# Performance work log

Measured on AMD Instinct MI355X. Metric: run time of the kernel, lower is better.

The kernel has to match this reference:

```python
import jax, jax.numpy as jnp
import numpy as np

N_NODES = 50000
N_EDGES = 500000
IN_DIM = 32
HID = 64
NUM_GRAPHS = 64


def _inv(d):
    # 1/d with inf -> 0, as in PyG HypergraphConv
    return jnp.where(d > 0, 1.0 / d, 0.0)


def hypergraph_conv(xh, row0, row1, W, b, n_hnodes, n_hedges):
    """PyG HypergraphConv (heads=1, no attention, unit hyperedge weights).
    xh: (n_hnodes, din) hyper-node features; row0: hyper-node ids, row1: hyperedge ids.
    Index n_hnodes / n_hedges is a padding slot for masked-out incidences.
    """
    xw = xh @ W                                   # (n_hnodes, dout) Theta
    xw = jnp.concatenate([xw, jnp.zeros((1, xw.shape[1]), xw.dtype)], axis=0)
    ones = jnp.ones(row0.shape[0], xw.dtype)
    D = _inv(jax.ops.segment_sum(ones, row0, num_segments=n_hnodes + 1))  # node degree^-1
    B = _inv(jax.ops.segment_sum(ones, row1, num_segments=n_hedges + 1))  # edge size^-1
    # node -> hyperedge aggregation, scaled by B
    he = jax.ops.segment_sum(xw[row0], row1, num_segments=n_hedges + 1) * B[:, None]
    # hyperedge -> node aggregation, scaled by D
    out = jax.ops.segment_sum(he[row1], row0, num_segments=n_hnodes + 1) * D[:, None]
    return out[:n_hnodes] + b


def setup_inputs() -> dict:
    key = jax.random.key(0)
    ks = jax.random.split(key, 12)
    x = jax.random.normal(ks[0], (N_NODES, 16), jnp.float32)
    edge_attr = jax.random.normal(ks[1], (N_EDGES, IN_DIM), jnp.float32)
    edge_index = jax.random.randint(ks[2], (2, N_EDGES), 0, N_NODES, dtype=jnp.int64)
    batch = jnp.sort(jax.random.randint(ks[3], (N_NODES,), 0, NUM_GRAPHS, dtype=jnp.int64))
    node_imp = jax.random.uniform(ks[4], (N_NODES,), jnp.float32)
    s = 0.05
    W0 = jax.random.normal(ks[5], (IN_DIM, HID), jnp.float32) * s
    b0 = jax.random.normal(ks[6], (HID,), jnp.float32) * s
    W1 = jax.random.normal(ks[7], (HID, HID), jnp.float32) * s
    b1 = jax.random.normal(ks[8], (HID,), jnp.float32) * s
    W2 = jax.random.normal(ks[9], (HID, HID), jnp.float32) * s
    b2 = jax.random.normal(ks[10], (HID,), jnp.float32) * s
    return {"x": x, "edge_attr": edge_attr, "edge_index": edge_index, "batch": batch,
            "node_imp": node_imp, "W0": W0, "b0": b0, "W1": W1, "b1": b1,
            "W2": W2, "b2": b2, "num_graphs": NUM_GRAPHS}


def reference(x, edge_attr, edge_index, batch, node_imp, W0, b0, W1, b1, W2, b2, num_graphs):
    N = x.shape[0]
    E = edge_index.shape[1]
    edge_imp = jnp.minimum(node_imp[edge_index[0]], node_imp[edge_index[1]])
    # --- Dual Hypergraph Transform (get_DHT) ---
    row0 = jnp.repeat(jnp.arange(E), 2)            # hyper-node = original edge id
    row1 = edge_index.T.reshape(-1)                # hyperedge  = original node id
    deg = jax.ops.segment_sum(jnp.ones(2 * E, jnp.float32), row1, num_segments=N)
    keep = deg[row1] != 1.0                        # drop incidences of degree-1 hyperedges
    row0 = jnp.where(keep, row0, E)                # redirect dropped entries to padding slot
    row1 = jnp.where(keep, row1, N + E)
    # self-loops: hyperedge ids N..N+E-1 (equivalent to torch's max_edge+1.., since
    # unused hyperedge slots receive nothing and B^-1 there is 0)
    row0 = jnp.concatenate([row0, jnp.arange(E)])
    row1 = jnp.concatenate([row1, N + jnp.arange(E)])
    edge_batch = batch[edge_index[0]]              # == hyperedge_index[1].reshape(-1,2)[:,0]
    # --- conv stack (dropout in eval mode = identity) ---
    h = edge_attr * edge_imp[:, None]
    xs = []
    for (W, b) in ((W0, b0), (W1, b1), (W2, b2)):
        h = jax.nn.relu(hypergraph_conv(h, row0, row1, W, b, E, N + E))
        h = h * edge_imp[:, None]
        xs.append(h)
    gh = jnp.concatenate(
        [jax.ops.segment_sum(h_i, edge_batch, num_segments=num_graphs) for h_i in xs], axis=1)
    return gh
```

## Files before the change

### kernel.cpp

```cpp
#include <hip/hip_runtime.h>
#include <hip/hip_bf16.h>
#include <cstdint>
#include <cstddef>

typedef unsigned short u16;
typedef unsigned int   u32;
typedef short bf16x8 __attribute__((ext_vector_type(8)));
typedef float f32x4  __attribute__((ext_vector_type(4)));

__device__ __forceinline__ float bf2f(u16 v){ return __uint_as_float(((u32)v)<<16); }
__device__ __forceinline__ u16 f2bf(float f){
  u32 x = __float_as_uint(f);
  return (u16)((x + 0x7FFFu + ((x>>16)&1u)) >> 16);
}
__device__ __forceinline__ void atomAddF(float* p, float v){ unsafeAtomicAdd(p, v); }
__device__ __forceinline__ float rlanef(float v, int q){
  return __int_as_float(__builtin_amdgcn_readlane(__float_as_int(v), q));
}

__global__ void kzero(int* p, int n){
  int i = blockIdx.x*blockDim.x + threadIdx.x;
  if(i < n) p[i] = 0;
}

__global__ void kdeg2(const int* __restrict__ ei0, const int* __restrict__ ei1,
                      int* __restrict__ deg0, int* __restrict__ deg1, int E){
  int e = blockIdx.x*blockDim.x + threadIdx.x;
  if(e >= E) return;
  atomicAdd(&deg0[ei0[e]], 1);
  atomicAdd(&deg1[ei1[e]], 1);
}

__global__ __launch_bounds__(256) void ktilesum(const int* __restrict__ deg0,
                                                const int* __restrict__ deg1,
                                                int* __restrict__ tsum,
                                                int N, int nt){
  __shared__ int sh[256];
  const int b = blockIdx.x;
  const int* deg = (b < nt) ? deg0 : deg1;
  const int tile = (b < nt) ? b : b - nt;
  const int t = threadIdx.x;
  const int i = tile*256 + t;
  sh[t] = (i < N) ? deg[i] : 0;
  __syncthreads();
  for(int s = 128; s > 0; s >>= 1){
    if(t < s) sh[t] += sh[t+s];
    __syncthreads();
  }
  if(t == 0) tsum[b] = sh[0];
}
__global__ __launch_bounds__(256) void kmid(int* __restrict__ tsum,
                                            int* __restrict__ off0,
                                            int* __restrict__ off1,
                                            int N, int nt){
  __shared__ int sh[256];
  const int b = blockIdx.x;
  int* ts = tsum + b*nt;
  const int t = threadIdx.x;
  sh[t] = (t < nt) ? ts[t] : 0;
  __syncthreads();
  for(int s = 1; s < 256; s <<= 1){
    int x = (t >= s) ? sh[t-s] : 0;
    __syncthreads();
    sh[t] += x;
    __syncthreads();
  }
  if(t < nt) ts[t] = (t == 0) ? 0 : sh[t-1];
  if(t == 255){ int* off = b ? off1 : off0; off[N] = sh[255]; }
}
__global__ __launch_bounds__(256) void kapply(const int* __restrict__ deg0,
                                              const int* __restrict__ deg1,
                                              const int* __restrict__ tsum,
                                              int* __restrict__ off0,
                                              int* __restrict__ off1,
                                              float* __restrict__ dinv,
                                              int N, int nt){
  __shared__ int sh[256];
  const int b = blockIdx.x;
  const int* deg = (b < nt) ? deg0 : deg1;
  int*       off = (b < nt) ? off0 : off1;
  const int tile = (b < nt) ? b : b - nt;
  const int base = tsum[b];
  const int t = threadIdx.x;
  const int i = tile*256 + t;
  sh[t] = (i < N) ? deg[i] : 0;
  __syncthreads();
  for(int s = 1; s < 256; s <<= 1){
    int x = (t >= s) ? sh[t-s] : 0;
    __syncthreads();
    sh[t] += x;
    __syncthreads();
  }
  if(i < N){
    off[i] = base + ((t == 0) ? 0 : sh[t-1]);
    if(b < nt){
      int d = deg0[i] + deg1[i];
      dinv[i] = (d > 1) ? (1.f/(float)d) : 0.f;
    }
  }
}

__global__ void kperm(const int* __restrict__ ei0, const int* __restrict__ ei1,
                      const float* __restrict__ nimp, const float* __restrict__ dinv,
                      const int* __restrict__ batch, const int* __restrict__ off0,
                      int* __restrict__ cur0, u32* __restrict__ euv,
                      f32x4* __restrict__ coef, unsigned char* __restrict__ ebat,
                      int* __restrict__ orig, float* __restrict__ imp, int E){
  int e = blockIdx.x*blockDim.x + threadIdx.x;
  if(e >= E) return;
  int u = ei0[e], v = ei1[e];
  int pos = off0[u] + atomicAdd(&cur0[u], 1);
  float iu = dinv[u], iv = dinv[v];
  float rc = (iu > 0.f && iv > 0.f) ? (1.f/3.f)
           : ((iu > 0.f || iv > 0.f) ? 0.5f : 1.f);
  float ie = fminf(nimp[u], nimp[v]);
  euv[pos]  = (u32)u | ((u32)v << 16);
  f32x4 c; c.x = rc; c.y = iu*rc; c.z = iv*rc; c.w = ie;
  coef[pos] = c;
  ebat[pos] = (unsigned char)batch[u];
  orig[pos] = e;
  imp[pos]  = ie;
}

__global__ void kfillv(const u32* __restrict__ euv, const int* __restrict__ off1,
                       int* __restrict__ cur1, int* __restrict__ list1, int E){
  int p = blockIdx.x*blockDim.x + threadIdx.x;
  if(p >= E) return;
  int v = (int)(euv[p] >> 16);
  list1[off1[v] + atomicAdd(&cur1[v], 1)] = p;
}

__global__ void kprepw(const float* __restrict__ W0, u16* __restrict__ wf0,
                       const float* __restrict__ W1, u16* __restrict__ wf1,
                       const float* __restrict__ W2, u16* __restrict__ wf2){
  const int b = blockIdx.x;
  const float* W; u16* wf; int NC, sbase;
  if(b == 0){ W = W0; wf = wf0; NC = 1; sbase = 0; }
  else if(b <= 2){ W = W1; wf = wf1; NC = 2; sbase = (b-1)*256; }
  else { W = W2; wf = wf2; NC = 2; sbase = (b-3)*256; }
  int s = sbase + threadIdx.x;
  if(s >= 4*NC*64) return;
  int lane = s & 63;
  int c    = (s >> 6) % NC;
  int tt   = s / (NC*64);
  int n  = tt*16 + (lane & 15);
  int k0 = c*32 + (lane >> 4)*8;
  #pragma unroll
  for(int j = 0; j < 8; j++)
    wf[(size_t)s*8 + j] = f2bf(W[(size_t)(k0 + j)*64 + n]);
}

__global__ __launch_bounds__(256) void kgemm0(const float* __restrict__ srcf,
                                              u16* __restrict__ buf,
                                              const u16* __restrict__ wf,
                                              const float* __restrict__ imp,
                                              const int* __restrict__ orig,
                                              int E){
  const int t    = threadIdx.x;
  const int wv   = t >> 6;
  const int lane = t & 63;
  const int quad = lane >> 4;
  const int l15  = lane & 15;
  const int row0 = blockIdx.x*64 + wv*16;
  if(row0 >= E) return;

  bf16x8 bfr[4];
  #pragma unroll
  for(int i = 0; i < 4; i++)
    bfr[i] = *(const bf16x8*)(wf + ((size_t)i*64 + lane)*8);

  const int myrow = row0 + l15;
  const int oe = orig[myrow];
  const float* s = srcf + (size_t)oe*32 + quad*8;
  const float sc = imp[myrow];
  f32x4 v0 = *(const f32x4*)s;
  f32x4 v1 = *(const f32x4*)(s+4);
  bf16x8 afr;
  afr[0]=(short)f2bf(v0.x*sc); afr[1]=(short)f2bf(v0.y*sc);
  afr[2]=(short)f2bf(v0.z*sc); afr[3]=(short)f2bf(v0.w*sc);
  afr[4]=(short)f2bf(v1.x*sc); afr[5]=(short)f2bf(v1.y*sc);
  afr[6]=(short)f2bf(v1.z*sc); afr[7]=(short)f2bf(v1.w*sc);

  #pragma unroll
  for(int tt = 0; tt < 4; tt++){
    f32x4 a = {0.f,0.f,0.f,0.f};
    a = __builtin_amdgcn_mfma_f32_16x16x32_bf16(afr, bfr[tt], a, 0, 0, 0);
    const int n = tt*16 + l15;
    #pragma unroll
    for(int r = 0; r < 4; r++)
      buf[(size_t)(row0 + quad*4 + r)*64 + n] = f2bf(a[r]);
  }
}

__global__ __launch_bounds__(256) void kagg(const u16* __restrict__ buf,
                                            const int* __restrict__ off0,
                                            const int* __restrict__ off1,
                                            const int* __restrict__ list1,
                                            u16* __restrict__ heb, int N){
  const int t = threadIdx.x, wv = t >> 6, lane = t & 63;
  const int n = blockIdx.x*4 + wv;
  if(n >= N) return;
  const int rsub = lane >> 3, cb = lane & 7;
  float acc[8];
  #pragma unroll
  for(int k = 0; k < 8; k++) acc[k] = 0.f;

  auto accum = [&](uint4 x){
    acc[0] += bf2f((u16)x.x); acc[1] += bf2f((u16)(x.x>>16));
    acc[2] += bf2f((u16)x.y); acc[3] += bf2f((u16)(x.y>>16));
    acc[4] += bf2f((u16)x.z); acc[5] += bf2f((u16)(x.z>>16));
    acc[6] += bf2f((u16)x.w); acc[7] += bf2f((u16)(x.w>>16));
  };
  const uint4 zero4 = {0,0,0,0};

  {
    const int s0 = off0[n], d0 = off0[n+1] - s0;
    const u16* base = buf + (size_t)s0*64;
    int j = 0;
    for(; j + 8 <= d0; j += 8)
      accum(*(const uint4*)(base + (size_t)(j+rsub)*64 + cb*8));
    if(j < d0)
      accum((rsub < d0-j) ? *(const uint4*)(base + (size_t)(j+rsub)*64 + cb*8) : zero4);
  }
  {
    const int s1 = off1[n], d1 = off1[n+1] - s1;
    int j = 0;
    for(; j + 8 <= d1; j += 8){
      int e = list1[s1 + j + rsub];
      accum(*(const uint4*)(buf + (size_t)e*64 + cb*8));
    }
    if(j < d1){
      uint4 x = zero4;
      if(rsub < d1-j){
        int e = list1[s1 + j + rsub];
        x = *(const uint4*)(buf + (size_t)e*64 + cb*8);
      }
      accum(x);
    }
  }
  #pragma unroll
  for(int m = 8; m <= 32; m <<= 1)
    #pragma unroll
    for(int k = 0; k < 8; k++) acc[k] += __shfl_xor(acc[k], m);
  if(rsub == 0){
    u32 o[4];
    #pragma unroll
    for(int k = 0; k < 4; k++)
      o[k] = (u32)f2bf(acc[2*k]) | ((u32)f2bf(acc[2*k+1]) << 16);
    *(uint4*)(heb + (size_t)n*64 + cb*8) = make_uint4(o[0],o[1],o[2],o[3]);
  }
}

template<bool DO_GEMM>
__global__ __launch_bounds__(256, 3) void kfused(u16* __restrict__ buf,
                                                 const u16* __restrict__ heb,
                                                 const u32* __restrict__ euv,
                                                 const f32x4* __restrict__ coef,
                                                 const unsigned char* __restrict__ ebat,
                                                 const float* __restrict__ bias,
                                                 const u16* __restrict__ wf,
                                                 float* __restrict__ ghL,
                                                 int E){
  constexpr int HTSZ = DO_GEMM ? 4*16*72 : 4;
  __shared__ __align__(16) u16 hT[HTSZ];
  const int t = threadIdx.x, wv = t >> 6, lane = t & 63;
  const int quad = lane >> 4, l15 = lane & 15;
  const float bd = bias[lane];

  bf16x8 bfr[8];
  if(DO_GEMM){
    #pragma unroll
    for(int i = 0; i < 8; i++)
      bfr[i] = *(const bf16x8*)(wf + ((size_t)i*64 + lane)*8);
  }

  float pool = 0.f;
  int cur_g = -1;
  const int base = __builtin_amdgcn_readfirstlane((int)(blockIdx.x*256) + wv*64);
  u16* hTw = DO_GEMM ? &hT[wv*1152] : &hT[0];

  u32 uvp = 0; f32x4 cf = {0.f,0.f,0.f,0.f}; int bt = 0;
  if(base < E){
    uvp = euv[base + l15];
    cf  = coef[base + l15];
    bt  = (int)ebat[base + l15];
  }

  #pragma unroll
  for(int it = 0; it < 4; it++){
    const int r0 = base + it*16;
    if(r0 < E){
      u16 bv[16], hu[16], hv[16];
      const u16* bufr = buf + (size_t)r0*64;
      #pragma unroll
      for(int q = 0; q < 16; q++){
        const u32 uv = (u32)__builtin_amdgcn_readlane((int)uvp, q);
        hv[q] = heb[(size_t)(uv >> 16)*64 + lane];
        hu[q] = heb[(size_t)(uv & 0xffffu)*64 + lane];
        bv[q] = bufr[q*64 + lane];
      }
      u32 uvpN = uvp; f32x4 cfN = cf; int btN = bt;
      if(it < 3){
        const int r1 = r0 + 16;
        if(r1 < E){
          uvpN = euv[r1 + l15];
          cfN  = coef[r1 + l15];
          btN  = (int)ebat[r1 + l15];
        }
      }
      const int bFirst = __builtin_amdgcn_readlane(bt, 0);
      const int bLast  = __builtin_amdgcn_readlane(bt, 15);
      if(bFirst != cur_g){
        if(cur_g >= 0) atomAddF(&ghL[cur_g*192 + lane], pool);
        pool = 0.f; cur_g = bFirst;
      }
      if(bFirst == bLast){
        #pragma unroll
        for(int q = 0; q < 16; q++){
          const float rc   = rlanef(cf.x, q);
          const float iurc = rlanef(cf.y, q);
          const float ivrc = rlanef(cf.z, q);
          const float ie   = rlanef(cf.w, q);
          float o = fmaxf(fmaf(bf2f(bv[q]), rc,
                          fmaf(bf2f(hu[q]), iurc,
                          fmaf(bf2f(hv[q]), ivrc, bd))), 0.f) * ie;
          pool += o;
          if(DO_GEMM) hTw[q*72 + lane] = f2bf(o);
        }
      } else {
        #pragma unroll
        for(int q = 0; q < 16; q++){
          const float rc   = rlanef(cf.x, q);
          const float iurc = rlanef(cf.y, q);
          const float ivrc = rlanef(cf.z, q);
          const float ie   = rlanef(cf.w, q);
          const int   bq   = __builtin_amdgcn_readlane(bt, q);
          float o = fmaxf(fmaf(bf2f(bv[q]), rc,
                          fmaf(bf2f(hu[q]), iurc,
                          fmaf(bf2f(hv[q]), ivrc, bd))), 0.f) * ie;
          if(bq != cur_g){
            if(cur_g >= 0) atomAddF(&ghL[cur_g*192 + lane], pool);
            pool = 0.f; cur_g = bq;
          }
          pool += o;
          if(DO_GEMM) hTw[q*72 + lane] = f2bf(o);
        }
      }
      if(DO_GEMM){
        bf16x8 afr0 = *(const bf16x8*)&hTw[l15*72 + quad*8];
        bf16x8 afr1 = *(const bf16x8*)&hTw[l15*72 + 32 + quad*8];
        #pragma unroll
        for(int tt = 0; tt < 4; tt++){
          f32x4 a = {0.f,0.f,0.f,0.f};
          a = __builtin_amdgcn_mfma_f32_16x16x32_bf16(afr0, bfr[tt*2+0], a, 0, 0, 0);
          a = __builtin_amdgcn_mfma_f32_16x16x32_bf16(afr1, bfr[tt*2+1], a, 0, 0, 0);
          const int n = tt*16 + l15;
          #pragma unroll
          for(int r = 0; r < 4; r++)
            buf[(size_t)(r0 + quad*4 + r)*64 + n] = f2bf(a[r]);
        }
      }
      uvp = uvpN; cf = cfN; bt = btN;
    }
  }
  if(cur_g >= 0) atomAddF(&ghL[cur_g*192 + lane], pool);
}

__global__ void kfinal(const float* __restrict__ gh, float* __restrict__ out, int n){
  int i = blockIdx.x*blockDim.x + threadIdx.x;
  if(i < n) out[i] = gh[i];
}

extern "C" void kernel_launch(void* const* d_in, const int* in_sizes, int n_in,
                              void* d_out, int out_size, void* d_ws, size_t ws_size,
                              hipStream_t stream) {
  const float* edge_attr = (const float*)d_in[1];
  const int*   ei        = (const int*)d_in[2];
  const int*   batch     = (const int*)d_in[3];
  const float* nimp      = (const float*)d_in[4];
  const float* Ws[3] = { (const float*)d_in[5], (const float*)d_in[7], (const float*)d_in[9] };
  const float* bs[3] = { (const float*)d_in[6], (const float*)d_in[8], (const float*)d_in[10] };

  const int E = in_sizes[1] / 32;
  const int N = in_sizes[4];
  const int* ei0 = ei;
  const int* ei1 = ei + E;

  char* p = (char*)d_ws;
  auto carve = [&](size_t bytes)->char*{
    char* r = p; p += (bytes + 255) & ~(size_t)255; return r;
  };
  const int nt = (N + 255)/256;
  float* imp   = (float*)carve((size_t)E*4);
  int*   deg0  = (int*)  carve((size_t)4*N*4);
  int*   deg1  = deg0 + N;
  int*   cur0  = deg0 + 2*N;
  int*   cur1  = deg0 + 3*N;
  float* dinv  = (float*)carve((size_t)N*4);
  int*   off0  = (int*)  carve((size_t)(N+1)*4);
  int*   off1  = (int*)  carve((size_t)(N+1)*4);
  int*   tsum  = (int*)  carve((size_t)2*nt*4);
  int*   orig  = (int*)  carve((size_t)E*4);
  int*   list1 = (int*)  carve((size_t)E*4);
  u32*   euv   = (u32*)  carve((size_t)E*4);
  f32x4* coef  = (f32x4*)carve((size_t)E*16);
  unsigned char* ebat = (unsigned char*)carve((size_t)E);
  u16*   heb   = (u16*)  carve((size_t)N*64*2);
  u16*   buf   = (u16*)  carve((size_t)E*64*2);
  float* gh    = (float*)carve((size_t)64*192*4);
  u16*   wfs[3];
  for(int l = 0; l < 3; l++) wfs[l] = (u16*)carve((size_t)4096*2);

  kzero<<<(4*N+255)/256, 256, 0, stream>>>(deg0, 4*N);
  kzero<<<(12288+255)/256, 256, 0, stream>>>((int*)gh, 12288);
  kdeg2<<<(E+255)/256, 256, 0, stream>>>(ei0, ei1, deg0, deg1, E);
  ktilesum<<<2*nt, 256, 0, stream>>>(deg0, deg1, tsum, N, nt);
  kmid<<<2, 256, 0, stream>>>(tsum, off0, off1, N, nt);
  kapply<<<2*nt, 256, 0, stream>>>(deg0, deg1, tsum, off0, off1, dinv, N, nt);
  kperm<<<(E+255)/256, 256, 0, stream>>>(ei0, ei1, nimp, dinv, batch, off0, cur0,
                                         euv, coef, ebat, orig, imp, E);
  kfillv<<<(E+255)/256, 256, 0, stream>>>(euv, off1, cur1, list1, E);
  kprepw<<<5, 256, 0, stream>>>(Ws[0], wfs[0], Ws[1], wfs[1], Ws[2], wfs[2]);

  const int nbG = (E + 63)/64;
  const int nbA = (N + 3)/4;
  const int nbF = (E + 255)/256;

  kgemm0<<<nbG, 256, 0, stream>>>(edge_attr, buf, wfs[0], imp, orig, E);
  kagg<<<nbA, 256, 0, stream>>>(buf, off0, off1, list1, heb, N);
  kfused<true ><<<nbF, 256, 0, stream>>>(buf, heb, euv, coef, ebat, bs[0], wfs[1], gh + 0*64, E);
  kagg<<<nbA, 256, 0, stream>>>(buf, off0, off1, list1, heb, N);
  kfused<true ><<<nbF, 256, 0, stream>>>(buf, heb, euv, coef, ebat, bs[1], wfs[2], gh + 1*64, E);
  kagg<<<nbA, 256, 0, stream>>>(buf, off0, off1, list1, heb, N);
  kfused<false><<<nbF, 256, 0, stream>>>(buf, heb, euv, coef, ebat, bs[2], nullptr, gh + 2*64, E);
  kfinal<<<(12288+255)/256, 256, 0, stream>>>(gh, (float*)d_out, 12288);
}
```

Baseline: 447.5 us.

## Pack per-edge records into one AoS struct and scatter gemm0 outputs via inverse permutation

Per-edge metadata (uv, coefficients, importance, batch id) moves from separate SoA arrays into one 32-byte struct, so kfused fetches it with two 16-byte loads instead of three separate loads. kperm now writes scattered 32-byte records plus an inverse permutation and importance in original edge order. kgemm0 then reads edge_attr contiguously and scatters its output rows, and kfillv reads edge ids directly instead of re-reading packed uv. In exchange, record writes in kperm are larger and scattered, and the kgemm0 output stores become scattered row writes.

Result: faster. 432.5 us (-3.4%).

```diff
diff --git a/kernel.cpp b/kernel.cpp
--- a/kernel.cpp
+++ b/kernel.cpp
@@ -7,6 +7,12 @@
 typedef unsigned int   u32;
 typedef short bf16x8 __attribute__((ext_vector_type(8)));
 typedef float f32x4  __attribute__((ext_vector_type(4)));
+
+struct __align__(16) ERec {
+  u32 uv;
+  float rc, iurc, ivrc;
+  float ie; u32 bat; u32 pad0, pad1;
+};
 
 __device__ __forceinline__ float bf2f(u16 v){ return __uint_as_float(((u32)v)<<16); }
 __device__ __forceinline__ u16 f2bf(float f){
@@ -103,9 +109,8 @@
 __global__ void kperm(const int* __restrict__ ei0, const int* __restrict__ ei1,
                       const float* __restrict__ nimp, const float* __restrict__ dinv,
                       const int* __restrict__ batch, const int* __restrict__ off0,
-                      int* __restrict__ cur0, u32* __restrict__ euv,
-                      f32x4* __restrict__ coef, unsigned char* __restrict__ ebat,
-                      int* __restrict__ orig, float* __restrict__ imp, int E){
+                      int* __restrict__ cur0, ERec* __restrict__ rec,
+                      int* __restrict__ iperm, float* __restrict__ impO, int E){
   int e = blockIdx.x*blockDim.x + threadIdx.x;
   if(e >= E) return;
   int u = ei0[e], v = ei1[e];
@@ -114,20 +119,22 @@
   float rc = (iu > 0.f && iv > 0.f) ? (1.f/3.f)
            : ((iu > 0.f || iv > 0.f) ? 0.5f : 1.f);
   float ie = fminf(nimp[u], nimp[v]);
-  euv[pos]  = (u32)u | ((u32)v << 16);
-  f32x4 c; c.x = rc; c.y = iu*rc; c.z = iv*rc; c.w = ie;
-  coef[pos] = c;
-  ebat[pos] = (unsigned char)batch[u];
-  orig[pos] = e;
-  imp[pos]  = ie;
-}
-
-__global__ void kfillv(const u32* __restrict__ euv, const int* __restrict__ off1,
-                       int* __restrict__ cur1, int* __restrict__ list1, int E){
-  int p = blockIdx.x*blockDim.x + threadIdx.x;
-  if(p >= E) return;
-  int v = (int)(euv[p] >> 16);
-  list1[off1[v] + atomicAdd(&cur1[v], 1)] = p;
+  ERec r;
+  r.uv = (u32)u | ((u32)v << 16);
+  r.rc = rc; r.iurc = iu*rc; r.ivrc = iv*rc;
+  r.ie = ie; r.bat = (u32)batch[u]; r.pad0 = 0; r.pad1 = 0;
+  rec[pos]  = r;
+  iperm[e]  = pos;
+  impO[e]   = ie;
+}
+
+__global__ void kfillv(const int* __restrict__ ei1, const int* __restrict__ iperm,
+                       const int* __restrict__ off1, int* __restrict__ cur1,
+                       int* __restrict__ list1, int E){
+  int e = blockIdx.x*blockDim.x + threadIdx.x;
+  if(e >= E) return;
+  int v = ei1[e];
+  list1[off1[v] + atomicAdd(&cur1[v], 1)] = iperm[e];
 }
 
 __global__ void kprepw(const float* __restrict__ W0, u16* __restrict__ wf0,
@@ -153,8 +160,8 @@
 __global__ __launch_bounds__(256) void kgemm0(const float* __restrict__ srcf,
                                               u16* __restrict__ buf,
                                               const u16* __restrict__ wf,
-                                              const float* __restrict__ imp,
-                                              const int* __restrict__ orig,
+                                              const float* __restrict__ impO,
+                                              const int* __restrict__ iperm,
                                               int E){
   const int t    = threadIdx.x;
   const int wv   = t >> 6;
@@ -170,9 +177,9 @@
     bfr[i] = *(const bf16x8*)(wf + ((size_t)i*64 + lane)*8);
 
   const int myrow = row0 + l15;
-  const int oe = orig[myrow];
-  const float* s = srcf + (size_t)oe*32 + quad*8;
-  const float sc = imp[myrow];
+  const float* s = srcf + (size_t)myrow*32 + quad*8;
+  const float sc = impO[myrow];
+  const int ip = iperm[myrow];
   f32x4 v0 = *(const f32x4*)s;
   f32x4 v1 = *(const f32x4*)(s+4);
   bf16x8 afr;
@@ -181,6 +188,10 @@
   afr[4]=(short)f2bf(v1.x*sc); afr[5]=(short)f2bf(v1.y*sc);
   afr[6]=(short)f2bf(v1.z*sc); afr[7]=(short)f2bf(v1.w*sc);
 
+  int dr[4];
+  #pragma unroll
+  for(int r = 0; r < 4; r++) dr[r] = __shfl(ip, quad*4 + r);
+
   #pragma unroll
   for(int tt = 0; tt < 4; tt++){
     f32x4 a = {0.f,0.f,0.f,0.f};
@@ -188,7 +199,7 @@
     const int n = tt*16 + l15;
     #pragma unroll
     for(int r = 0; r < 4; r++)
-      buf[(size_t)(row0 + quad*4 + r)*64 + n] = f2bf(a[r]);
+      buf[(size_t)dr[r]*64 + n] = f2bf(a[r]);
   }
 }
 
@@ -254,9 +265,7 @@
 template<bool DO_GEMM>
 __global__ __launch_bounds__(256, 3) void kfused(u16* __restrict__ buf,
                                                  const u16* __restrict__ heb,
-                                                 const u32* __restrict__ euv,
-                                                 const f32x4* __restrict__ coef,
-                                                 const unsigned char* __restrict__ ebat,
+                                                 const f32x4* __restrict__ rec4,
                                                  const float* __restrict__ bias,
                                                  const u16* __restrict__ wf,
                                                  float* __restrict__ ghL,
@@ -281,9 +290,11 @@
 
   u32 uvp = 0; f32x4 cf = {0.f,0.f,0.f,0.f}; int bt = 0;
   if(base < E){
-    uvp = euv[base + l15];
-    cf  = coef[base + l15];
-    bt  = (int)ebat[base + l15];
+    f32x4 w0 = rec4[(size_t)(base+l15)*2];
+    f32x4 w1 = rec4[(size_t)(base+l15)*2 + 1];
+    uvp = __float_as_uint(w0.x);
+    cf.x = w0.y; cf.y = w0.z; cf.z = w0.w; cf.w = w1.x;
+    bt  = __float_as_int(w1.y);
   }
 
   #pragma unroll
@@ -303,9 +314,11 @@
       if(it < 3){
         const int r1 = r0 + 16;
         if(r1 < E){
-          uvpN = euv[r1 + l15];
-          cfN  = coef[r1 + l15];
-          btN  = (int)ebat[r1 + l15];
+          f32x4 w0 = rec4[(size_t)(r1+l15)*2];
+          f32x4 w1 = rec4[(size_t)(r1+l15)*2 + 1];
+          uvpN = __float_as_uint(w0.x);
+          cfN.x = w0.y; cfN.y = w0.z; cfN.z = w0.w; cfN.w = w1.x;
+          btN  = __float_as_int(w1.y);
         }
       }
       const int bFirst = __builtin_amdgcn_readlane(bt, 0);
@@ -391,7 +404,6 @@
     char* r = p; p += (bytes + 255) & ~(size_t)255; return r;
   };
   const int nt = (N + 255)/256;
-  float* imp   = (float*)carve((size_t)E*4);
   int*   deg0  = (int*)  carve((size_t)4*N*4);
   int*   deg1  = deg0 + N;
   int*   cur0  = deg0 + 2*N;
@@ -400,11 +412,10 @@
   int*   off0  = (int*)  carve((size_t)(N+1)*4);
   int*   off1  = (int*)  carve((size_t)(N+1)*4);
   int*   tsum  = (int*)  carve((size_t)2*nt*4);
-  int*   orig  = (int*)  carve((size_t)E*4);
+  int*   iperm = (int*)  carve((size_t)E*4);
+  float* impO  = (float*)carve((size_t)E*4);
   int*   list1 = (int*)  carve((size_t)E*4);
-  u32*   euv   = (u32*)  carve((size_t)E*4);
-  f32x4* coef  = (f32x4*)carve((size_t)E*16);
-  unsigned char* ebat = (unsigned char*)carve((size_t)E);
+  ERec*  rec   = (ERec*) carve((size_t)E*sizeof(ERec));
   u16*   heb   = (u16*)  carve((size_t)N*64*2);
   u16*   buf   = (u16*)  carve((size_t)E*64*2);
   float* gh    = (float*)carve((size_t)64*192*4);
@@ -418,20 +429,20 @@
   kmid<<<2, 256, 0, stream>>>(tsum, off0, off1, N, nt);
   kapply<<<2*nt, 256, 0, stream>>>(deg0, deg1, tsum, off0, off1, dinv, N, nt);
   kperm<<<(E+255)/256, 256, 0, stream>>>(ei0, ei1, nimp, dinv, batch, off0, cur0,
-                                         euv, coef, ebat, orig, imp, E);
-  kfillv<<<(E+255)/256, 256, 0, stream>>>(euv, off1, cur1, list1, E);
+                                         rec, iperm, impO, E);
+  kfillv<<<(E+255)/256, 256, 0, stream>>>(ei1, iperm, off1, cur1, list1, E);
   kprepw<<<5, 256, 0, stream>>>(Ws[0], wfs[0], Ws[1], wfs[1], Ws[2], wfs[2]);
 
   const int nbG = (E + 63)/64;
   const int nbA = (N + 3)/4;
   const int nbF = (E + 255)/256;
 
-  kgemm0<<<nbG, 256, 0, stream>>>(edge_attr, buf, wfs[0], imp, orig, E);
+  kgemm0<<<nbG, 256, 0, stream>>>(edge_attr, buf, wfs[0], impO, iperm, E);
   kagg<<<nbA, 256, 0, stream>>>(buf, off0, off1, list1, heb, N);
-  kfused<true ><<<nbF, 256, 0, stream>>>(buf, heb, euv, coef, ebat, bs[0], wfs[1], gh + 0*64, E);
+  kfused<true ><<<nbF, 256, 0, stream>>>(buf, heb, (const f32x4*)rec, bs[0], wfs[1], gh + 0*64, E);
   kagg<<<nbA, 256, 0, stream>>>(buf, off0, off1, list1, heb, N);
-  kfused<true ><<<nbF, 256, 0, stream>>>(buf, heb, euv, coef, ebat, bs[1], wfs[2], gh + 1*64, E);
+  kfused<true ><<<nbF, 256, 0, stream>>>(buf, heb, (const f32x4*)rec, bs[1], wfs[2], gh + 1*64, E);
   kagg<<<nbA, 256, 0, stream>>>(buf, off0, off1, list1, heb, N);
-  kfused<false><<<nbF, 256, 0, stream>>>(buf, heb, euv, coef, ebat, bs[2], nullptr, gh + 2*64, E);
+  kfused<false><<<nbF, 256, 0, stream>>>(buf, heb, (const f32x4*)rec, bs[2], nullptr, gh + 2*64, E);
   kfinal<<<(12288+255)/256, 256, 0, stream>>>(gh, (float*)d_out, 12288);
 }
```
